# Performance work log

Hardware: AMD Instinct MI355X
Metric: run time of the kernel (lower is better)

Reference implementation:

```python
import jax, jax.numpy as jnp
import numpy as np


def setup_inputs() -> dict:
    key = jax.random.key(0)
    k1, k2, k3 = jax.random.split(key, 3)
    b, d, h, w = 16, 64, 32, 32
    n = b * h * w  # 16384
    x = jax.random.normal(k1, (b, d, h, w), dtype=jnp.float32)
    mu = jax.random.normal(k2, (n, d), dtype=jnp.float32)
    logvar = jax.random.normal(k3, (n, d), dtype=jnp.float32)
    return {"x": x, "mu": mu, "logvar": logvar}


def reference(x, mu, logvar):
    # x: (b, d, h, w) -> (N, d) with N = b*h*w
    b, d, h, w = x.shape
    flat_x = jnp.transpose(x, (0, 2, 3, 1)).reshape(-1, d)  # (N, d)

    inv_v = jnp.exp(-logvar)  # (N, d), 1/var

    # pos[i] = -0.5 * sum_d (x_i - mu_i)^2 / var_i
    pos = -0.5 * jnp.sum(jnp.square(flat_x - mu) * inv_v, axis=-1)  # (N,)

    # neg[i] = -0.5 * mean_j sum_d (x_j - mu_i)^2 / var_i
    # Expand the square so we never materialize the (N, N, d) tensor:
    #   sum_d (x_j - mu_i)^2 / v_i = x_j^2 . inv_v_i - 2 x_j . (mu_i*inv_v_i) + sum_d mu_i^2 * inv_v_i
    x2 = jnp.square(flat_x)                          # (N, d)
    mu_inv_v = mu * inv_v                            # (N, d)
    c = jnp.sum(jnp.square(mu) * inv_v, axis=-1)     # (N,)
    # D[i, j]: (N, N) pairwise weighted sq-distance
    D = jnp.einsum('id,jd->ij', inv_v, x2) - 2.0 * jnp.einsum('id,jd->ij', mu_inv_v, flat_x) + c[:, None]
    neg = -0.5 * jnp.mean(D, axis=-1)                # (N,)

    loss = pos - neg
    return jnp.mean(loss)  # reduction='mean'
```

## Files before the change

### kernel.cpp

```cpp
#include <hip/hip_runtime.h>


#define NROWS 16384
#define DDIM  64
#define GRID  256
#define NCOL  258
#define NREP  4

__device__ double g_acc[NREP * NCOL];
__device__ int    g_counter = 0;

__global__ __launch_bounds__(256) void club_fused(const float* __restrict__ x,
                                                  const float* __restrict__ mu,
                                                  const float* __restrict__ logvar,
                                                  float* __restrict__ out) {
    __shared__ float  xt[64 * 65];
    __shared__ double red[256];
    __shared__ double S[NCOL];
    __shared__ int    is_last;

    const int tid = threadIdx.x;
    const int bid = blockIdx.x;
    const int i0  = bid * 64;
    const int b   = i0 >> 10;
    const int hw0 = i0 & 1023;

    const float* xb = x + (size_t)b * 65536 + hw0;
    #pragma unroll
    for (int t = tid; t < 1024; t += 256) {
        const int dd = t >> 4, j4 = (t & 15) * 4;
        const float4 v = *(const float4*)(xb + (size_t)dd * 1024 + j4);
        float* p = &xt[dd * 65 + j4];
        p[0] = v.x; p[1] = v.y; p[2] = v.z; p[3] = v.w;
    }
    __syncthreads();

    const int d  = tid & 63;
    const int j0 = (tid >> 6) * 16;
    double a_x = 0.0, a_x2 = 0.0, a_iv = 0.0, a_miv = 0.0, a_c = 0.0, a_pos = 0.0;
    const int base_idx = (i0 + j0) * DDIM + d;
    #pragma unroll
    for (int k = 0; k < 16; ++k) {
        const float xv = xt[d * 65 + j0 + k];
        const float m  = mu[base_idx + k * DDIM];
        const float lv = logvar[base_idx + k * DDIM];
        const float iv = expf(-lv);
        const float t2 = xv - m;
        a_x   += (double)xv;
        a_x2  += (double)(xv * xv);
        a_iv  += (double)iv;
        a_miv += (double)(m * iv);
        a_c   += (double)(m * m * iv);
        a_pos += (double)(t2 * t2 * iv);
    }

    double* acc = g_acc + (size_t)(bid & (NREP - 1)) * NCOL;

    #define VR(val, base)                                                              \
        red[tid] = (val); __syncthreads();                                             \
        if (tid < 64) atomicAdd(&acc[(base) + tid],                                    \
            red[tid] + red[tid + 64] + red[tid + 128] + red[tid + 192]);               \
        __syncthreads();
    VR(a_x,   0)
    VR(a_x2,  64)
    VR(a_iv,  128)
    VR(a_miv, 192)
    #undef VR

    red[tid] = a_c; __syncthreads();
    if (tid < 64) {
        double s = red[tid] + red[tid + 64] + red[tid + 128] + red[tid + 192];
        #pragma unroll
        for (int off = 32; off > 0; off >>= 1) s += __shfl_down(s, off, 64);
        if (tid == 0) atomicAdd(&acc[256], s);
    }
    __syncthreads();
    red[tid] = a_pos; __syncthreads();
    if (tid < 64) {
        double s = red[tid] + red[tid + 64] + red[tid + 128] + red[tid + 192];
        #pragma unroll
        for (int off = 32; off > 0; off >>= 1) s += __shfl_down(s, off, 64);
        if (tid == 0) atomicAdd(&acc[257], s);
    }

    asm volatile("s_waitcnt vmcnt(0)" ::: "memory");
    __syncthreads();
    if (tid == 0) {
        is_last = (atomicAdd(&g_counter, 1) == GRID - 1);
        if (is_last) atomicExch(&g_counter, 0);
    }
    __syncthreads();
    if (!is_last) return;

    for (int c = tid; c < NCOL; c += 256) {
        double s = 0.0;
        #pragma unroll
        for (int r = 0; r < NREP; ++r) {
            s += __hip_atomic_load(&g_acc[r * NCOL + c],
                                   __ATOMIC_RELAXED, __HIP_MEMORY_SCOPE_AGENT);
            __hip_atomic_store(&g_acc[r * NCOL + c], 0.0,
                               __ATOMIC_RELAXED, __HIP_MEMORY_SCOPE_AGENT);
        }
        S[c] = s;
    }
    __syncthreads();

    if (tid < 64) {
        double term = S[128 + tid] * S[64 + tid] - 2.0 * S[192 + tid] * S[tid];
        #pragma unroll
        for (int off = 32; off > 0; off >>= 1) term += __shfl_down(term, off, 64);
        if (tid == 0) {
            const double Nd   = (double)NROWS;
            const double sumD = term + Nd * S[256];
            out[0] = (float)(-0.5 / Nd * S[257] + 0.5 / (Nd * Nd) * sumD);
        }
    }
}

extern "C" void kernel_launch(void* const* d_in, const int* in_sizes, int n_in,
                              void* d_out, int out_size, void* d_ws, size_t ws_size,
                              hipStream_t stream) {
    const float* x      = (const float*)d_in[0];
    const float* mu     = (const float*)d_in[1];
    const float* logvar = (const float*)d_in[2];
    float* out = (float*)d_out;

    club_fused<<<GRID, 256, 0, stream>>>(x, mu, logvar, out);
}
```

Before: 17.58 us.

## Double grid to 512 blocks, vectorize mu/logvar loads, reduce via wave shuffles

Each block now handles 32 rows instead of 64, giving 512 blocks. The x tile is transposed into shared memory so threads read float4 of mu, logvar and x along the feature dimension. The per-block reduction becomes wave-level shuffles plus a single shared-memory pass with one barrier, replacing the previous five barrier-separated reductions. The number of global accumulator replicas grows to 8 to spread atomic contention. The intent is more parallelism to hide memory latency, wider loads and fewer synchronizations, at the cost of twice as many global atomics overall.

```diff
diff --git a/kernel.cpp b/kernel.cpp
--- a/kernel.cpp
+++ b/kernel.cpp
@@ -3,9 +3,10 @@
 
 #define NROWS 16384
 #define DDIM  64
-#define GRID  256
+#define GRID  512
+#define ROWS  32
 #define NCOL  258
-#define NREP  4
+#define NREP  8
 
 __device__ double g_acc[NREP * NCOL];
 __device__ int    g_counter = 0;
@@ -14,73 +15,99 @@
                                                   const float* __restrict__ mu,
                                                   const float* __restrict__ logvar,
                                                   float* __restrict__ out) {
-    __shared__ float  xt[64 * 65];
-    __shared__ double red[256];
+    __shared__ __align__(16) float xt[ROWS * 68];
+    __shared__ double red[64 * 16];
+    __shared__ double sred[8];
     __shared__ double S[NCOL];
     __shared__ int    is_last;
 
     const int tid = threadIdx.x;
     const int bid = blockIdx.x;
-    const int i0  = bid * 64;
+    const int i0  = bid * ROWS;
     const int b   = i0 >> 10;
     const int hw0 = i0 & 1023;
 
     const float* xb = x + (size_t)b * 65536 + hw0;
     #pragma unroll
-    for (int t = tid; t < 1024; t += 256) {
-        const int dd = t >> 4, j4 = (t & 15) * 4;
+    for (int c = 0; c < 2; ++c) {
+        const int f  = tid + 256 * c;
+        const int dd = f >> 3, j4 = (f & 7) * 4;
         const float4 v = *(const float4*)(xb + (size_t)dd * 1024 + j4);
-        float* p = &xt[dd * 65 + j4];
-        p[0] = v.x; p[1] = v.y; p[2] = v.z; p[3] = v.w;
+        xt[(j4 + 0) * 68 + dd] = v.x;
+        xt[(j4 + 1) * 68 + dd] = v.y;
+        xt[(j4 + 2) * 68 + dd] = v.z;
+        xt[(j4 + 3) * 68 + dd] = v.w;
     }
     __syncthreads();
 
-    const int d  = tid & 63;
-    const int j0 = (tid >> 6) * 16;
-    double a_x = 0.0, a_x2 = 0.0, a_iv = 0.0, a_miv = 0.0, a_c = 0.0, a_pos = 0.0;
-    const int base_idx = (i0 + j0) * DDIM + d;
+    const int q  = tid & 15;
+    const int rw = tid >> 4;
+
+    double ax[4]  = {0,0,0,0}, ax2[4]  = {0,0,0,0};
+    double aiv[4] = {0,0,0,0}, amiv[4] = {0,0,0,0};
+    double ac = 0.0, apos = 0.0;
+
     #pragma unroll
-    for (int k = 0; k < 16; ++k) {
-        const float xv = xt[d * 65 + j0 + k];
-        const float m  = mu[base_idx + k * DDIM];
-        const float lv = logvar[base_idx + k * DDIM];
-        const float iv = expf(-lv);
-        const float t2 = xv - m;
-        a_x   += (double)xv;
-        a_x2  += (double)(xv * xv);
-        a_iv  += (double)iv;
-        a_miv += (double)(m * iv);
-        a_c   += (double)(m * m * iv);
-        a_pos += (double)(t2 * t2 * iv);
+    for (int c = 0; c < 2; ++c) {
+        const int r = rw + 16 * c;
+        const float4 xv4 = *(const float4*)(&xt[r * 68 + 4 * q]);
+        const float4 m4  = *(const float4*)(mu     + (size_t)(i0 + r) * DDIM + 4 * q);
+        const float4 l4  = *(const float4*)(logvar + (size_t)(i0 + r) * DDIM + 4 * q);
+        const float xs[4] = {xv4.x, xv4.y, xv4.z, xv4.w};
+        const float ms[4] = {m4.x,  m4.y,  m4.z,  m4.w};
+        const float ls[4] = {l4.x,  l4.y,  l4.z,  l4.w};
+        #pragma unroll
+        for (int i = 0; i < 4; ++i) {
+            const float iv = expf(-ls[i]);
+            const float t2 = xs[i] - ms[i];
+            ax[i]   += (double)xs[i];
+            ax2[i]  += (double)(xs[i] * xs[i]);
+            aiv[i]  += (double)iv;
+            amiv[i] += (double)(ms[i] * iv);
+            ac      += (double)(ms[i] * ms[i] * iv);
+            apos    += (double)(t2 * t2 * iv);
+        }
     }
 
+    #pragma unroll
+    for (int i = 0; i < 4; ++i) {
+        ax[i]   += __shfl_xor(ax[i],   16, 64);  ax[i]   += __shfl_xor(ax[i],   32, 64);
+        ax2[i]  += __shfl_xor(ax2[i],  16, 64);  ax2[i]  += __shfl_xor(ax2[i],  32, 64);
+        aiv[i]  += __shfl_xor(aiv[i],  16, 64);  aiv[i]  += __shfl_xor(aiv[i],  32, 64);
+        amiv[i] += __shfl_xor(amiv[i], 16, 64);  amiv[i] += __shfl_xor(amiv[i], 32, 64);
+    }
+    #pragma unroll
+    for (int off = 1; off < 64; off <<= 1) {
+        ac   += __shfl_xor(ac,   off, 64);
+        apos += __shfl_xor(apos, off, 64);
+    }
+
+    const int wave = tid >> 6;
+    const int lane = tid & 63;
+    if (lane < 16) {
+        double* rp = &red[(wave * 16 + lane) * 16];
+        #pragma unroll
+        for (int i = 0; i < 4; ++i) {
+            rp[0 * 4 + i] = ax[i];  rp[1 * 4 + i] = ax2[i];
+            rp[2 * 4 + i] = aiv[i]; rp[3 * 4 + i] = amiv[i];
+        }
+    }
+    if (lane == 0) { sred[wave * 2] = ac; sred[wave * 2 + 1] = apos; }
+    __syncthreads();
+
     double* acc = g_acc + (size_t)(bid & (NREP - 1)) * NCOL;
-
-    #define VR(val, base)                                                              \
-        red[tid] = (val); __syncthreads();                                             \
-        if (tid < 64) atomicAdd(&acc[(base) + tid],                                    \
-            red[tid] + red[tid + 64] + red[tid + 128] + red[tid + 192]);               \
-        __syncthreads();
-    VR(a_x,   0)
-    VR(a_x2,  64)
-    VR(a_iv,  128)
-    VR(a_miv, 192)
-    #undef VR
-
-    red[tid] = a_c; __syncthreads();
     if (tid < 64) {
-        double s = red[tid] + red[tid + 64] + red[tid + 128] + red[tid + 192];
+        const int qq = tid >> 2, sub = tid & 3;
         #pragma unroll
-        for (int off = 32; off > 0; off >>= 1) s += __shfl_down(s, off, 64);
-        if (tid == 0) atomicAdd(&acc[256], s);
-    }
-    __syncthreads();
-    red[tid] = a_pos; __syncthreads();
-    if (tid < 64) {
-        double s = red[tid] + red[tid + 64] + red[tid + 128] + red[tid + 192];
-        #pragma unroll
-        for (int off = 32; off > 0; off >>= 1) s += __shfl_down(s, off, 64);
-        if (tid == 0) atomicAdd(&acc[257], s);
+        for (int s = 0; s < 4; ++s) {
+            double v = 0.0;
+            #pragma unroll
+            for (int W = 0; W < 4; ++W) v += red[(W * 16 + qq) * 16 + s * 4 + sub];
+            atomicAdd(&acc[s * 64 + tid], v);
+        }
+    } else if (tid == 64) {
+        atomicAdd(&acc[256], sred[0] + sred[2] + sred[4] + sred[6]);
+        atomicAdd(&acc[257], sred[1] + sred[3] + sred[5] + sred[7]);
     }
 
     asm volatile("s_waitcnt vmcnt(0)" ::: "memory");
```

Result: slower. 22.47 us (+27.8%).
